# Kernel tuning notes

Measured on AMD Instinct MI355X. Metric: run time of the kernel, lower is better.

The kernel has to match this reference:

```python
import jax, jax.numpy as jnp
import numpy as np

D_MODEL = 512
N_HEAD = 8


def setup_inputs() -> dict:
    key = jax.random.key(0)
    ks = jax.random.split(key, 9)
    s = 1.0 / np.sqrt(D_MODEL)
    inp = {
        "x": jax.random.normal(ks[0], (2, 4096, D_MODEL), dtype=jnp.float32),
        "wq": jax.random.uniform(ks[1], (D_MODEL, D_MODEL), jnp.float32, -s, s),
        "bq": jax.random.uniform(ks[2], (D_MODEL,), jnp.float32, -s, s),
        "wk": jax.random.uniform(ks[3], (D_MODEL, D_MODEL), jnp.float32, -s, s),
        "bk": jax.random.uniform(ks[4], (D_MODEL,), jnp.float32, -s, s),
        "wv": jax.random.uniform(ks[5], (D_MODEL, D_MODEL), jnp.float32, -s, s),
        "bv": jax.random.uniform(ks[6], (D_MODEL,), jnp.float32, -s, s),
        "wo": jax.random.uniform(ks[7], (D_MODEL, D_MODEL), jnp.float32, -s, s),
        "bo": jax.random.uniform(ks[8], (D_MODEL,), jnp.float32, -s, s),
    }
    return inp


def reference(x, wq, bq, wk, bk, wv, bv, wo, bo):
    B, S, D = x.shape
    H = N_HEAD
    Dh = D // H

    def split_heads(t):  # [B,S,D] -> [B,H,S,Dh]
        return t.reshape(B, S, H, Dh).transpose(0, 2, 1, 3)

    q = split_heads(x @ wq.T + bq)
    k = split_heads(x @ wk.T + bk)
    v = split_heads(x @ wv.T + bv)

    # explicit (unfused) attention, matching the torch module
    score = jnp.einsum("bhsd,bhtd->bhst", q, k) / jnp.sqrt(jnp.float32(Dh))
    attn = jax.nn.softmax(score, axis=-1)
    out = jnp.einsum("bhst,bhtd->bhsd", attn, v)  # [B,H,S,Dh]

    out = out.transpose(0, 2, 1, 3).reshape(B, S, D)
    return out @ wo.T + bo
```

## Files before the change

kernel.cpp:

```cpp
#include <hip/hip_runtime.h>
#include <math.h>

#define S_LEN 4096
#define DMODEL 512
#define NHEAD 8
#define E_ELEMS ((size_t)8192 * 512)
#define QSCALE 0.18033688f

typedef __attribute__((ext_vector_type(8))) short bf16x8;
typedef __attribute__((ext_vector_type(4))) float f32x4;
typedef __attribute__((ext_vector_type(16))) float f32x16;
typedef unsigned short u16;
typedef unsigned int u32;

__device__ __forceinline__ u16 f2bf(float f) {
    u32 u = __float_as_uint(f);
    u += 0x7FFFu + ((u >> 16) & 1u);
    return (u16)(u >> 16);
}
__device__ __forceinline__ float bf2f(u16 h) {
    return __uint_as_float((u32)h << 16);
}

#define MFMA16(a, b, c) __builtin_amdgcn_mfma_f32_16x16x32_bf16((a), (b), (c), 0, 0, 0)
#define MFMA32(a, b, c) __builtin_amdgcn_mfma_f32_32x32x16_bf16((a), (b), (c), 0, 0, 0)

__global__ __launch_bounds__(256) void cvt_all(
    const float* __restrict__ x,
    const float* __restrict__ wq, const float* __restrict__ wk,
    const float* __restrict__ wv, const float* __restrict__ wo,
    u16* __restrict__ xbf, u16* __restrict__ oq, u16* __restrict__ ok,
    u16* __restrict__ ov, u16* __restrict__ oo)
{
    const int bid = blockIdx.x;
    if (bid < 4096) {
        const int i = bid * 256 + threadIdx.x;
        const float4 v = ((const float4*)x)[i];
        uint2 hp;
        hp.x = (u32)f2bf(v.x) | ((u32)f2bf(v.y) << 16);
        hp.y = (u32)f2bf(v.z) | ((u32)f2bf(v.w) << 16);
        ((uint2*)xbf)[i] = hp;
    } else {
        const int i = (bid - 4096) * 256 + threadIdx.x;
        {
            const float4 v = ((const float4*)wq)[i];
            uint2 hp;
            hp.x = (u32)f2bf(v.x * QSCALE) | ((u32)f2bf(v.y * QSCALE) << 16);
            hp.y = (u32)f2bf(v.z * QSCALE) | ((u32)f2bf(v.w * QSCALE) << 16);
            ((uint2*)oq)[i] = hp;
        }
        {
            const float4 v = ((const float4*)wk)[i];
            uint2 hp;
            hp.x = (u32)f2bf(v.x) | ((u32)f2bf(v.y) << 16);
            hp.y = (u32)f2bf(v.z) | ((u32)f2bf(v.w) << 16);
            ((uint2*)ok)[i] = hp;
        }
        {
            const float4 v = ((const float4*)wv)[i];
            uint2 hp;
            hp.x = (u32)f2bf(v.x) | ((u32)f2bf(v.y) << 16);
            hp.y = (u32)f2bf(v.z) | ((u32)f2bf(v.w) << 16);
            ((uint2*)ov)[i] = hp;
        }
        {
            const float4 v = ((const float4*)wo)[i];
            uint2 hp;
            hp.x = (u32)f2bf(v.x) | ((u32)f2bf(v.y) << 16);
            hp.y = (u32)f2bf(v.z) | ((u32)f2bf(v.w) << 16);
            ((uint2*)oo)[i] = hp;
        }
    }
}

template<int MODE>
__global__ __launch_bounds__(256) void proj2_kernel(
    const u16* __restrict__ Abf,
    const u16* __restrict__ W0, const float* __restrict__ Bi0,
    const u16* __restrict__ W1, const float* __restrict__ Bi1,
    const u16* __restrict__ W2, const float* __restrict__ Bi2,
    u16* __restrict__ Qo, u16* __restrict__ Ko, u16* __restrict__ Vt,
    float* __restrict__ Out)
{
    __shared__ __align__(16) u16 sm[18432];
    u16* As = sm;
    u16* Bs = sm + 8192;

    const int tid = threadIdx.x;
    const int w = tid >> 6, l = tid & 63, g = (l >> 4), c = l & 15;
    const int wr = w >> 1, wc = w & 1;
    const int bm = blockIdx.x * 128;
    const int n0 = blockIdx.y * 128;
    const int z = (MODE == 0) ? blockIdx.z : 0;
    const u16* W   = (z == 0) ? W0 : (z == 1) ? W1 : W2;
    const float* Bi = (z == 0) ? Bi0 : (z == 1) ? Bi1 : Bi2;
    const float bsc = (MODE == 0 && z == 0) ? QSCALE : 1.0f;

    const int sr = l >> 3;
    const int slot = l & 7;

    f32x4 acc[4][4];
    #pragma unroll
    for (int i = 0; i < 4; ++i)
        #pragma unroll
        for (int j = 0; j < 4; ++j) acc[i][j] = (f32x4){0.f, 0.f, 0.f, 0.f};

    #pragma unroll 1
    for (int kt = 0; kt < 8; ++kt) {
        const int k0 = kt * 64;
        __syncthreads();
        #pragma unroll
        for (int i = 0; i < 4; ++i) {
            const int row = i * 32 + w * 8 + sr;
            const int scol = (slot ^ (row & 7)) * 8;
            __builtin_amdgcn_global_load_lds(
                Abf + (size_t)(bm + row) * DMODEL + k0 + scol,
                As + (i * 32 + w * 8) * 64, 16, 0, 0);
            __builtin_amdgcn_global_load_lds(
                W + (size_t)(n0 + row) * DMODEL + k0 + scol,
                Bs + (i * 32 + w * 8) * 64, 16, 0, 0);
        }
        __syncthreads();

        #pragma unroll
        for (int kc = 0; kc < 2; ++kc) {
            bf16x8 a[4], b[4];
            #pragma unroll
            for (int mf = 0; mf < 4; ++mf) {
                const int ra = wr * 64 + mf * 16 + c;
                a[mf] = *(const bf16x8*)(As + ra * 64 + (((kc * 4 + g) ^ (ra & 7)) * 8));
            }
            #pragma unroll
            for (int nf = 0; nf < 4; ++nf) {
                const int rb = wc * 64 + nf * 16 + c;
                b[nf] = *(const bf16x8*)(Bs + rb * 64 + (((kc * 4 + g) ^ (rb & 7)) * 8));
            }
            #pragma unroll
            for (int mf = 0; mf < 4; ++mf)
                #pragma unroll
                for (int nf = 0; nf < 4; ++nf)
                    acc[mf][nf] = MFMA16(a[mf], b[nf], acc[mf][nf]);
        }
    }

    if (MODE == 0 && z == 2) {
        __syncthreads();
        float* scr = (float*)sm;
        const int d = tid & 63, sb = tid >> 6;
        const int b = bm >> 12;
        #pragma unroll
        for (int pass = 0; pass < 2; ++pass) {
            if (wc == pass) {
                #pragma unroll
                for (int mf = 0; mf < 4; ++mf)
                    #pragma unroll
                    for (int nf = 0; nf < 4; ++nf) {
                        const float bias = Bi[n0 + pass * 64 + nf * 16 + c];
                        #pragma unroll
                        for (int r = 0; r < 4; ++r)
                            scr[(wr * 64 + mf * 16 + 4 * g + r) * 72 + nf * 16 + c] =
                                acc[mf][nf][r] + bias;
                    }
            }
            __syncthreads();
            const int hh = (n0 >> 6) + pass;
            const size_t obase =
                ((size_t)((b * NHEAD + hh) * 64 + d)) * S_LEN + (bm & (S_LEN - 1)) + sb * 32;
            u16 th[32];
            #pragma unroll
            for (int j = 0; j < 32; ++j)
                th[j] = f2bf(scr[(sb * 32 + j) * 72 + d]);
            #pragma unroll
            for (int q4 = 0; q4 < 4; ++q4)
                *(uint4*)(Vt + obase + q4 * 8) = *(const uint4*)&th[q4 * 8];
            __syncthreads();
        }
        return;
    }

    #pragma unroll
    for (int mf = 0; mf < 4; ++mf)
        #pragma unroll
        for (int nf = 0; nf < 4; ++nf) {
            const int n = n0 + wc * 64 + nf * 16 + c;
            const float bias = Bi[n] * bsc;
            #pragma unroll
            for (int r = 0; r < 4; ++r) {
                const int m = bm + wr * 64 + mf * 16 + 4 * g + r;
                const float v = acc[mf][nf][r] + bias;
                if (MODE == 1) {
                    Out[(size_t)m * DMODEL + n] = v;
                } else {
                    const int b = m >> 12, s = m & (S_LEN - 1);
                    const int hh = n >> 6, dd = n & 63;
                    const size_t o = ((size_t)((b * NHEAD + hh) * S_LEN + s)) * 64 + dd;
                    if (z == 0) Qo[o] = f2bf(v);
                    else        Ko[o] = f2bf(v);
                }
            }
        }
}

__global__ __launch_bounds__(256, 2) void attn_kernel(
    const u16* __restrict__ Qb, const u16* __restrict__ Kb,
    const u16* __restrict__ Vt, u16* __restrict__ OpB, float* __restrict__ Lp)
{
    __shared__ __align__(16) u16 sm[16384];

    const int tid = threadIdx.x;
    const int w = tid >> 6, l = tid & 63;
    const int r0 = l & 31, hi = l >> 5;

    const int f = blockIdx.x;
    const int wg = (f & 7) * 128 + (f >> 3);
    const int bh = wg >> 6, kvq = (wg >> 4) & 3, qb = wg & 15;
    const int b = bh >> 3, h = bh & 7;

    const size_t hoff = (size_t)bh * S_LEN * 64;
    const int qw = qb * 256 + w * 64;
    const int kv0 = kvq * 1024;

    bf16x8 qf[2][4];
    #pragma unroll
    for (int qfi = 0; qfi < 2; ++qfi)
        #pragma unroll
        for (int kc = 0; kc < 4; ++kc)
            qf[qfi][kc] = *(const bf16x8*)(Qb + hoff +
                (size_t)(qw + qfi * 32 + r0) * 64 + kc * 16 + hi * 8);

    const int rbase = r0 * 64;
    int soff[4];
    #pragma unroll
    for (int j = 0; j < 4; ++j) soff[j] = ((2 * j + hi) ^ (r0 & 7)) * 8;

    const int srow0 = w * 16 + (l >> 3);
    const int slot  = l & 7;
    const int srow1 = srow0 + 8;
    const u16* srcK0 = Kb + hoff + (size_t)(kv0 + srow0) * 64 + ((slot ^ (srow0 & 7)) * 8);
    const u16* srcK1 = Kb + hoff + (size_t)(kv0 + srow1) * 64 + ((slot ^ (srow1 & 7)) * 8);
    const u16* srcV0 = Vt + ((size_t)bh * 64 + srow0) * S_LEN + kv0 + ((slot ^ (srow0 & 7)) * 8);
    const u16* srcV1 = Vt + ((size_t)bh * 64 + srow1) * S_LEN + kv0 + ((slot ^ (srow1 & 7)) * 8);

#define STAGE(bufb, t) do {                                                        \
        u16* kb_ = sm + (bufb) * 8192 + w * 1024;                                  \
        u16* vb_ = kb_ + 4096;                                                     \
        __builtin_amdgcn_global_load_lds(srcK0 + (size_t)(t) * 4096, kb_,       16, 0, 0); \
        __builtin_amdgcn_global_load_lds(srcK1 + (size_t)(t) * 4096, kb_ + 512, 16, 0, 0); \
        __builtin_amdgcn_global_load_lds(srcV0 + (size_t)(t) * 64,   vb_,       16, 0, 0); \
        __builtin_amdgcn_global_load_lds(srcV1 + (size_t)(t) * 64,   vb_ + 512, 16, 0, 0); \
    } while (0)

#define ZERO16 {0.f,0.f,0.f,0.f,0.f,0.f,0.f,0.f,0.f,0.f,0.f,0.f,0.f,0.f,0.f,0.f}
    f32x16 o00 = ZERO16, o01 = ZERO16, o10 = ZERO16, o11 = ZERO16;
    float lA = 0.f, lB = 0.f;

    STAGE(0, 0);
    __syncthreads();
    int buf = 0;

    #pragma unroll 1
    for (int t = 0; t < 16; ++t) {
        if (t + 1 < 16) STAGE(buf ^ 1, t + 1);

        const u16* Kb_s = sm + buf * 8192;
        const u16* Vb_s = Kb_s + 4096;

        #pragma unroll
        for (int kvf = 0; kvf < 2; ++kvf) {
            f32x16 sA = ZERO16, sB = ZERO16;
            __builtin_amdgcn_s_setprio(1);
            #pragma unroll
            for (int kc = 0; kc < 4; ++kc) {
                const bf16x8 k = *(const bf16x8*)(Kb_s + kvf * 2048 + rbase + soff[kc]);
                sA = MFMA32(k, qf[0][kc], sA);
                sB = MFMA32(k, qf[1][kc], sB);
            }
            __builtin_amdgcn_s_setprio(0);

            #pragma unroll
            for (int r = 0; r < 16; ++r) {
                sA[r] = __builtin_amdgcn_exp2f(sA[r]);
                sB[r] = __builtin_amdgcn_exp2f(sB[r]);
            }
            #pragma unroll
            for (int r = 0; r < 16; ++r) { lA += sA[r]; lB += sB[r]; }

            #pragma unroll
            for (int hf = 0; hf < 2; ++hf) {
                const int rb = hf * 8;
                const int idx = kvf * 2 + hf;
                u32 x0, y0, x1, y1;
                asm("v_cvt_pk_bf16_f32 %0, %1, %2" : "=v"(x0) : "v"(sA[rb+0]), "v"(sA[rb+1]));
                asm("v_cvt_pk_bf16_f32 %0, %1, %2" : "=v"(y0) : "v"(sA[rb+4]), "v"(sA[rb+5]));
                asm("v_cvt_pk_bf16_f32 %0, %1, %2" : "=v"(x1) : "v"(sA[rb+2]), "v"(sA[rb+3]));
                asm("v_cvt_pk_bf16_f32 %0, %1, %2" : "=v"(y1) : "v"(sA[rb+6]), "v"(sA[rb+7]));
                asm volatile("v_permlane32_swap_b32 %0, %1" : "+v"(x0), "+v"(y0));
                asm volatile("v_permlane32_swap_b32 %0, %1" : "+v"(x1), "+v"(y1));
                union { u32 u[4]; bf16x8 v; } PA;
                PA.u[0] = x0; PA.u[1] = x1; PA.u[2] = y0; PA.u[3] = y1;
                asm("v_cvt_pk_bf16_f32 %0, %1, %2" : "=v"(x0) : "v"(sB[rb+0]), "v"(sB[rb+1]));
                asm("v_cvt_pk_bf16_f32 %0, %1, %2" : "=v"(y0) : "v"(sB[rb+4]), "v"(sB[rb+5]));
                asm("v_cvt_pk_bf16_f32 %0, %1, %2" : "=v"(x1) : "v"(sB[rb+2]), "v"(sB[rb+3]));
                asm("v_cvt_pk_bf16_f32 %0, %1, %2" : "=v"(y1) : "v"(sB[rb+6]), "v"(sB[rb+7]));
                asm volatile("v_permlane32_swap_b32 %0, %1" : "+v"(x0), "+v"(y0));
                asm volatile("v_permlane32_swap_b32 %0, %1" : "+v"(x1), "+v"(y1));
                union { u32 u[4]; bf16x8 v; } PB;
                PB.u[0] = x0; PB.u[1] = x1; PB.u[2] = y0; PB.u[3] = y1;

                const bf16x8 v0 = *(const bf16x8*)(Vb_s + rbase + soff[idx]);
                const bf16x8 v1 = *(const bf16x8*)(Vb_s + 2048 + rbase + soff[idx]);
                __builtin_amdgcn_s_setprio(1);
                o00 = MFMA32(PA.v, v0, o00);
                o01 = MFMA32(PA.v, v1, o01);
                o10 = MFMA32(PB.v, v0, o10);
                o11 = MFMA32(PB.v, v1, o11);
                __builtin_amdgcn_s_setprio(0);
            }
        }

        __syncthreads();
        buf ^= 1;
    }
#undef STAGE

    lA += __shfl_xor(lA, 32);
    lB += __shfl_xor(lB, 32);
    if (hi == 0) {
        Lp[((size_t)kvq * 16 + bh) * S_LEN + qw + r0]      = lA;
        Lp[((size_t)kvq * 16 + bh) * S_LEN + qw + 32 + r0] = lB;
    }

    u16* Ob = OpB + (size_t)kvq * E_ELEMS + (size_t)b * S_LEN * DMODEL;
    #pragma unroll
    for (int qfi = 0; qfi < 2; ++qfi)
        #pragma unroll
        for (int df = 0; df < 2; ++df) {
            #pragma unroll
            for (int r = 0; r < 16; ++r) {
                const float ov = qfi ? (df ? o11[r] : o10[r]) : (df ? o01[r] : o00[r]);
                const int q = qfi * 32 + (r & 3) + 8 * (r >> 2) + 4 * hi;
                Ob[(size_t)(qw + q) * DMODEL + h * 64 + df * 32 + r0] = f2bf(ov);
            }
        }
}

__global__ __launch_bounds__(256) void combine_kernel(
    const u16* __restrict__ Op, const float* __restrict__ Lp,
    u16* __restrict__ A)
{
    const int i = blockIdx.x * 256 + threadIdx.x;
    const int m = i >> 6;
    const int col = (i & 63) * 8;
    const int b = m >> 12, s = m & (S_LEN - 1), h = col >> 6;
    const int bh = b * 8 + h;

    float lt = 0.f;
    #pragma unroll
    for (int kq = 0; kq < 4; ++kq)
        lt += Lp[((size_t)kq * 16 + bh) * S_LEN + s];
    const float inv = 1.0f / lt;

    float acc[8] = {};
    #pragma unroll
    for (int kq = 0; kq < 4; ++kq) {
        const uint4 v = *(const uint4*)(Op + (size_t)kq * E_ELEMS + (size_t)m * DMODEL + col);
        const u16* p = (const u16*)&v;
        #pragma unroll
        for (int j = 0; j < 8; ++j) acc[j] += bf2f(p[j]);
    }
    u16 r[8];
    #pragma unroll
    for (int j = 0; j < 8; ++j) r[j] = f2bf(acc[j] * inv);
    *(uint4*)(A + (size_t)m * DMODEL + col) = *(const uint4*)r;
}

extern "C" void kernel_launch(void* const* d_in, const int* in_sizes, int n_in,
                              void* d_out, int out_size, void* d_ws, size_t ws_size,
                              hipStream_t stream)
{
    const float* x  = (const float*)d_in[0];
    const float* wq = (const float*)d_in[1];
    const float* bq = (const float*)d_in[2];
    const float* wk = (const float*)d_in[3];
    const float* bk = (const float*)d_in[4];
    const float* wv = (const float*)d_in[5];
    const float* bv = (const float*)d_in[6];
    const float* wo = (const float*)d_in[7];
    const float* bo = (const float*)d_in[8];

    u16* ws = (u16*)d_ws;
    const size_t E = E_ELEMS;
    u16* xbf  = ws;
    u16* Qbf  = ws + E;
    u16* Kbf  = ws + 2 * E;
    u16* Vtbf = ws + 3 * E;
    u16* wqbf = ws + 4 * E;
    u16* wkbf = wqbf + DMODEL * DMODEL;
    u16* wvbf = wkbf + DMODEL * DMODEL;
    u16* wobf = wvbf + DMODEL * DMODEL;
    u16* OpB  = wobf + DMODEL * DMODEL;
    float* Lp = (float*)(OpB + 4 * E);

    cvt_all<<<dim3(4352), 256, 0, stream>>>(
        x, wq, wk, wv, wo, xbf, wqbf, wkbf, wvbf, wobf);

    proj2_kernel<0><<<dim3(64, 4, 3), 256, 0, stream>>>(
        xbf, wqbf, bq, wkbf, bk, wvbf, bv, Qbf, Kbf, Vtbf, nullptr);

    attn_kernel<<<dim3(1024), 256, 0, stream>>>(Qbf, Kbf, Vtbf, OpB, Lp);

    combine_kernel<<<dim3(2048), 256, 0, stream>>>(OpB, Lp, xbf);

    proj2_kernel<1><<<dim3(64, 4, 1), 256, 0, stream>>>(
        xbf, wobf, bo, nullptr, nullptr, nullptr, nullptr,
        nullptr, nullptr, nullptr, (float*)d_out);
}
```

Before: 130.5 us.

## Load K and V fragments directly from global memory instead of LDS staging

Removes the double-buffered LDS staging of K and V tiles (global_load_lds plus barriers) from the attention kernel. Each wave now reads its MFMA operand fragments straight from global memory, relying on L1/L2 caching because all four waves in a block read the same K/V tiles. This drops the LDS traffic and the per-iteration __syncthreads, but exposes global-load latency with no explicit prefetch and gives up in-block reuse through shared memory.

```diff
diff --git a/kernel.cpp b/kernel.cpp
--- a/kernel.cpp
+++ b/kernel.cpp
@@ -205,8 +205,6 @@
     const u16* __restrict__ Qb, const u16* __restrict__ Kb,
     const u16* __restrict__ Vt, u16* __restrict__ OpB, float* __restrict__ Lp)
 {
-    __shared__ __align__(16) u16 sm[16384];
-
     const int tid = threadIdx.x;
     const int w = tid >> 6, l = tid & 63;
     const int r0 = l & 31, hi = l >> 5;
@@ -228,50 +226,23 @@
             qf[qfi][kc] = *(const bf16x8*)(Qb + hoff +
                 (size_t)(qw + qfi * 32 + r0) * 64 + kc * 16 + hi * 8);
 
-    const int rbase = r0 * 64;
-    int soff[4];
-    #pragma unroll
-    for (int j = 0; j < 4; ++j) soff[j] = ((2 * j + hi) ^ (r0 & 7)) * 8;
-
-    const int srow0 = w * 16 + (l >> 3);
-    const int slot  = l & 7;
-    const int srow1 = srow0 + 8;
-    const u16* srcK0 = Kb + hoff + (size_t)(kv0 + srow0) * 64 + ((slot ^ (srow0 & 7)) * 8);
-    const u16* srcK1 = Kb + hoff + (size_t)(kv0 + srow1) * 64 + ((slot ^ (srow1 & 7)) * 8);
-    const u16* srcV0 = Vt + ((size_t)bh * 64 + srow0) * S_LEN + kv0 + ((slot ^ (srow0 & 7)) * 8);
-    const u16* srcV1 = Vt + ((size_t)bh * 64 + srow1) * S_LEN + kv0 + ((slot ^ (srow1 & 7)) * 8);
-
-#define STAGE(bufb, t) do {                                                        \
-        u16* kb_ = sm + (bufb) * 8192 + w * 1024;                                  \
-        u16* vb_ = kb_ + 4096;                                                     \
-        __builtin_amdgcn_global_load_lds(srcK0 + (size_t)(t) * 4096, kb_,       16, 0, 0); \
-        __builtin_amdgcn_global_load_lds(srcK1 + (size_t)(t) * 4096, kb_ + 512, 16, 0, 0); \
-        __builtin_amdgcn_global_load_lds(srcV0 + (size_t)(t) * 64,   vb_,       16, 0, 0); \
-        __builtin_amdgcn_global_load_lds(srcV1 + (size_t)(t) * 64,   vb_ + 512, 16, 0, 0); \
-    } while (0)
+    const u16* Kg = Kb + hoff + (size_t)(kv0 + r0) * 64 + hi * 8;
+    const u16* Vg0 = Vt + ((size_t)bh * 64 + r0) * S_LEN + kv0 + hi * 8;
+    const u16* Vg1 = Vg0 + (size_t)32 * S_LEN;
 
 #define ZERO16 {0.f,0.f,0.f,0.f,0.f,0.f,0.f,0.f,0.f,0.f,0.f,0.f,0.f,0.f,0.f,0.f}
     f32x16 o00 = ZERO16, o01 = ZERO16, o10 = ZERO16, o11 = ZERO16;
     float lA = 0.f, lB = 0.f;
 
-    STAGE(0, 0);
-    __syncthreads();
-    int buf = 0;
-
     #pragma unroll 1
     for (int t = 0; t < 16; ++t) {
-        if (t + 1 < 16) STAGE(buf ^ 1, t + 1);
-
-        const u16* Kb_s = sm + buf * 8192;
-        const u16* Vb_s = Kb_s + 4096;
-
         #pragma unroll
         for (int kvf = 0; kvf < 2; ++kvf) {
             f32x16 sA = ZERO16, sB = ZERO16;
             __builtin_amdgcn_s_setprio(1);
             #pragma unroll
             for (int kc = 0; kc < 4; ++kc) {
-                const bf16x8 k = *(const bf16x8*)(Kb_s + kvf * 2048 + rbase + soff[kc]);
+                const bf16x8 k = *(const bf16x8*)(Kg + (size_t)(t * 64 + kvf * 32) * 64 + kc * 16);
                 sA = MFMA32(k, qf[0][kc], sA);
                 sB = MFMA32(k, qf[1][kc], sB);
             }
@@ -288,7 +259,7 @@
             #pragma unroll
             for (int hf = 0; hf < 2; ++hf) {
                 const int rb = hf * 8;
-                const int idx = kvf * 2 + hf;
+                const int kvp = t * 64 + (kvf * 2 + hf) * 16;
                 u32 x0, y0, x1, y1;
                 asm("v_cvt_pk_bf16_f32 %0, %1, %2" : "=v"(x0) : "v"(sA[rb+0]), "v"(sA[rb+1]));
                 asm("v_cvt_pk_bf16_f32 %0, %1, %2" : "=v"(y0) : "v"(sA[rb+4]), "v"(sA[rb+5]));
@@ -307,8 +278,8 @@
                 union { u32 u[4]; bf16x8 v; } PB;
                 PB.u[0] = x0; PB.u[1] = x1; PB.u[2] = y0; PB.u[3] = y1;
 
-                const bf16x8 v0 = *(const bf16x8*)(Vb_s + rbase + soff[idx]);
-                const bf16x8 v1 = *(const bf16x8*)(Vb_s + 2048 + rbase + soff[idx]);
+                const bf16x8 v0 = *(const bf16x8*)(Vg0 + kvp);
+                const bf16x8 v1 = *(const bf16x8*)(Vg1 + kvp);
                 __builtin_amdgcn_s_setprio(1);
                 o00 = MFMA32(PA.v, v0, o00);
                 o01 = MFMA32(PA.v, v1, o01);
@@ -317,11 +288,7 @@
                 __builtin_amdgcn_s_setprio(0);
             }
         }
-
-        __syncthreads();
-        buf ^= 1;
-    }
-#undef STAGE
+    }
 
     lA += __shfl_xor(lA, 32);
     lB += __shfl_xor(lB, 32);
```

Result: slower. 183.3 us (+40.5%).
